# Performance work log

Measured on AMD Instinct MI355X. Metric: run time of the kernel, lower is better.

## Reference

```python
import jax, jax.numpy as jnp
import numpy as np

HEADS = 8
HEAD_DIM = 16
SCALE = HEAD_DIM ** -0.5
FIRE_RATE = 0.5
C = 128      # channel_n == embed_dim
MLP = 512


def layer_norm(x, s, b, eps=1e-5):
    m = jnp.mean(x, axis=-1, keepdims=True)
    v = jnp.mean((x - m) ** 2, axis=-1, keepdims=True)
    return (x - m) / jnp.sqrt(v + eps) * s + b


def pos_enc(H, W, D):
    # positional_encoding_3d(height, width, depth, dim=2): dim=2 path
    ph = jnp.arange(H, dtype=jnp.float32)
    pw = jnp.arange(W, dtype=jnp.float32)
    pd = jnp.arange(D, dtype=jnp.float32)
    # div terms: exp(0*-ln1e4/2)=1, exp(1*-ln1e4/2)=1e-2, exp(2*-ln1e4/2)=1e-4
    pe_h = jnp.stack([jnp.sin(ph * 1.0), jnp.cos(ph * 1.0)], -1)[:, None, None, :]
    pe_w = jnp.stack([jnp.sin(pw * 1e-2), jnp.cos(pw * 1e-2)], -1)[None, :, None, :]
    pe_d = jnp.stack([jnp.sin(pd * 1e-4), jnp.cos(pd * 1e-4)], -1)[None, None, :, :]
    return (pe_h + pe_w + pe_d).reshape(1, H * W * D, 2)


def localize(t, H, W, D):
    # t: [b, h, n, hd] -> gather zero-padded 3x3x3 neighbourhood -> [b, h, n, 27, hd]
    b, h, n, hd = t.shape
    v = t.reshape(b, h, H, W, D, hd)
    v = jnp.pad(v, ((0, 0), (0, 0), (1, 1), (1, 1), (1, 1), (0, 0)))
    shifts = [v[:, :, i:i + H, j:j + W, k:k + D, :]
              for i in range(3) for j in range(3) for k in range(3)]
    return jnp.stack(shifts, axis=-2).reshape(b, h, n, 27, hd)


def nca_step(x, params, key):
    (W_qkv, W_out, b_out, ln1_s, ln1_b, W_ff1, b_ff1, W_ff2, b_ff2,
     ln2_s, ln2_b, ln3_s, ln3_b, W_head, b_head) = params
    b, H, W, D, c = x.shape
    N = H * W * D
    xf = x.reshape(b, N, c)
    # overwrite last 2 channels with positional encoding
    pe = pos_enc(H, W, D)
    y = jnp.concatenate([xf[..., :-2], jnp.broadcast_to(pe, (b, N, 2))], axis=-1)
    # PreNorm localized attention
    yn = layer_norm(y, ln1_s, ln1_b)
    qkv = yn @ W_qkv                       # [b, N, 3*inner]
    q, k, v = jnp.split(qkv, 3, axis=-1)
    split = lambda t: t.reshape(b, N, HEADS, HEAD_DIM).transpose(0, 2, 1, 3)
    q, k, v = split(q), split(k), split(v)
    kl = localize(k, H, W, D)              # [b, h, N, 27, hd]
    vl = localize(v, H, W, D)
    dots = jnp.einsum('bhnd,bhnkd->bhnk', q, kl) * SCALE
    attn = jax.nn.softmax(dots, axis=-1)
    o = jnp.einsum('bhnk,bhnkd->bhnd', attn, vl)
    o = o.transpose(0, 2, 1, 3).reshape(b, N, HEADS * HEAD_DIM)
    y = o @ W_out + b_out + y
    # PreNorm feed-forward
    yn2 = layer_norm(y, ln2_s, ln2_b)
    ff = jax.nn.gelu(yn2 @ W_ff1 + b_ff1, approximate=False) @ W_ff2 + b_ff2
    y = ff + y
    # mlp head -> dx
    dx = layer_norm(y, ln3_s, ln3_b) @ W_head + b_head
    dx = dx.reshape(b, H, W, D, c)
    mask = (jax.random.uniform(key, (b, H, W, D, 1)) > FIRE_RATE).astype(x.dtype)
    return x + dx * mask


def setup_inputs() -> dict:
    key = jax.random.key(0)
    ks = jax.random.split(key, 8)
    s = 0.02
    inner = HEADS * HEAD_DIM
    return {
        'x': jax.random.normal(ks[0], (1, 24, 24, 24, C), jnp.float32),
        'W_qkv': jax.random.normal(ks[1], (C, 3 * inner), jnp.float32) * s,
        'W_out': jax.random.normal(ks[2], (inner, C), jnp.float32) * s,
        'b_out': jnp.zeros((C,), jnp.float32),
        'ln1_s': jnp.ones((C,), jnp.float32),
        'ln1_b': jnp.zeros((C,), jnp.float32),
        'W_ff1': jax.random.normal(ks[3], (C, MLP), jnp.float32) * s,
        'b_ff1': jnp.zeros((MLP,), jnp.float32),
        'W_ff2': jax.random.normal(ks[4], (MLP, C), jnp.float32) * s,
        'b_ff2': jnp.zeros((C,), jnp.float32),
        'ln2_s': jnp.ones((C,), jnp.float32),
        'ln2_b': jnp.zeros((C,), jnp.float32),
        'ln3_s': jnp.ones((C,), jnp.float32),
        'ln3_b': jnp.zeros((C,), jnp.float32),
        'W_head': jax.random.normal(ks[5], (C, C), jnp.float32) * s,
        'b_head': jnp.zeros((C,), jnp.float32),
        'steps': 2,
    }


def reference(x, W_qkv, W_out, b_out, ln1_s, ln1_b, W_ff1, b_ff1, W_ff2, b_ff2,
              ln2_s, ln2_b, ln3_s, ln3_b, W_head, b_head, steps):
    params = (W_qkv, W_out, b_out, ln1_s, ln1_b, W_ff1, b_ff1, W_ff2, b_ff2,
              ln2_s, ln2_b, ln3_s, ln3_b, W_head, b_head)
    key = jax.random.key(42)
    for s in range(steps):
        x = nca_step(x, params, jax.random.fold_in(key, s))
    return x
```

## Files before the change

### kernel.cpp

```cpp
#include <hip/hip_runtime.h>
#include <hip/hip_fp16.h>
#include <cstdint>
#include <cstddef>

#define NCELL 13824

typedef short bf16x8 __attribute__((ext_vector_type(8)));
typedef float f32x4  __attribute__((ext_vector_type(4)));
typedef _Float16 h2v __attribute__((ext_vector_type(2)));

__device__ __forceinline__ unsigned short f2bf(float x) {
  union { float f; uint32_t u; } c; c.f = x;
  uint32_t r = c.u + 0x7fffu + ((c.u >> 16) & 1u);
  return (unsigned short)(r >> 16);
}

__device__ __forceinline__ bf16x8 afrag_f32(const float* p) {
  float4 u0 = *(const float4*)p;
  float4 u1 = *(const float4*)(p + 4);
  bf16x8 a;
  a[0] = (short)f2bf(u0.x); a[1] = (short)f2bf(u0.y);
  a[2] = (short)f2bf(u0.z); a[3] = (short)f2bf(u0.w);
  a[4] = (short)f2bf(u1.x); a[5] = (short)f2bf(u1.y);
  a[6] = (short)f2bf(u1.z); a[7] = (short)f2bf(u1.w);
  return a;
}

__device__ __forceinline__ void ldh2x2(const __half* p, __half2& a, __half2& b) {
  uint2 u = *(const uint2*)p;
  union { uint32_t u; __half2 h; } c0, c1;
  c0.u = u.x; c1.u = u.y;
  a = c0.h; b = c1.h;
}

__device__ __forceinline__ float fdot2(__half2 a, __half2 b, float c) {
#if __has_builtin(__builtin_amdgcn_fdot2)
  union { __half2 h; h2v n; } ua, ub;
  ua.h = a; ub.h = b;
  return __builtin_amdgcn_fdot2(ua.n, ub.n, c, false);
#else
  __half2 d = __hmul2(a, b);
  return c + __low2float(d) + __high2float(d);
#endif
}

__device__ __forceinline__ float gelu_f(float x) {
  float u = 0.7978845608f * x * (1.f + 0.044715f * x * x);
  float e = __expf(2.f * u);
  float t = 1.f - 2.f / (e + 1.f);
  return 0.5f * x * (1.f + t);
}

__device__ __forceinline__ void tf2x32(uint32_t k0, uint32_t k1,
                                       uint32_t x0, uint32_t x1,
                                       uint32_t& o0, uint32_t& o1) {
  uint32_t k2 = k0 ^ k1 ^ 0x1BD11BDAu;
  x0 += k0; x1 += k1;
#define TFR(r) { x0 += x1; x1 = (x1 << (r)) | (x1 >> (32 - (r))); x1 ^= x0; }
  TFR(13) TFR(15) TFR(26) TFR(6)   x0 += k1; x1 += k2 + 1u;
  TFR(17) TFR(29) TFR(16) TFR(24)  x0 += k2; x1 += k0 + 2u;
  TFR(13) TFR(15) TFR(26) TFR(6)   x0 += k0; x1 += k1 + 3u;
  TFR(17) TFR(29) TFR(16) TFR(24)  x0 += k1; x1 += k2 + 4u;
  TFR(13) TFR(15) TFR(26) TFR(6)   x0 += k2; x1 += k0 + 5u;
#undef TFR
  o0 = x0; o1 = x1;
}

__device__ __forceinline__ float pe_val(int n, int c) {
  int dd = n % 24, ww = (n / 24) % 24, hh = n / 576;
  if (c == 126)
    return sinf((float)hh) + sinf(0.01f * (float)ww) + sinf(0.0001f * (float)dd);
  return cosf((float)hh) + cosf(0.01f * (float)ww) + cosf(0.0001f * (float)dd);
}

__device__ __forceinline__ void packOne(const float* __restrict__ W, int K, int N,
                                        unsigned short* __restrict__ P, int f) {
  int KT = K >> 5;
  int lane = f & 63;
  int ft = f >> 6;
  int kt = ft % KT, nt = ft / KT;
  int col = nt * 16 + (lane & 15);
  int k0 = kt * 32 + (lane >> 4) * 8;
  uint32_t w[4];
  #pragma unroll
  for (int p = 0; p < 4; ++p) {
    uint32_t lo = f2bf(W[(size_t)(k0 + 2 * p) * N + col]);
    uint32_t hi = f2bf(W[(size_t)(k0 + 2 * p + 1) * N + col]);
    w[p] = lo | (hi << 16);
  }
  uint4 v; v.x = w[0]; v.y = w[1]; v.z = w[2]; v.w = w[3];
  ((uint4*)P)[f] = v;
}

__global__ __launch_bounds__(256) void packAll(
    const float* __restrict__ Wqkv, const float* __restrict__ Wout,
    const float* __restrict__ Wff1, const float* __restrict__ Wff2,
    const float* __restrict__ Whead,
    unsigned short* __restrict__ pQkv, unsigned short* __restrict__ pOut,
    unsigned short* __restrict__ pFF1, unsigned short* __restrict__ pFF2,
    unsigned short* __restrict__ pHead) {
  int f = blockIdx.x * 256 + threadIdx.x;
  if (f < 6144)        packOne(Wqkv, 128, 384, pQkv, f);
  else if (f < 8192)   packOne(Wout, 128, 128, pOut, f - 6144);
  else if (f < 16384)  packOne(Wff1, 128, 512, pFF1, f - 8192);
  else if (f < 24576)  packOne(Wff2, 512, 128, pFF2, f - 16384);
  else if (f < 26624)  packOne(Whead, 128, 128, pHead, f - 24576);
}

__global__ __launch_bounds__(256) void nca_k1(
    const float* __restrict__ x, const float* __restrict__ ln1s,
    const float* __restrict__ ln1b, const unsigned short* __restrict__ pQkv,
    __half* __restrict__ wqkv,
    const int* __restrict__ steps, int s) {
  if (s >= *steps) return;
  __shared__ float ly[16][132];
  __shared__ float lmean[16], lrstd[16];
  const int t = threadIdx.x;
  const int swz = (blockIdx.x & 7) * 108 + (blockIdx.x >> 3);
  const int base = swz * 16;
  #pragma unroll
  for (int i = 0; i < 8; ++i) {
    int idx = i * 256 + t;
    int r = idx >> 7, c = idx & 127;
    int n = base + r;
    ly[r][c] = (c < 126) ? x[(size_t)n * 128 + c] : pe_val(n, c);
  }
  __syncthreads();
  { int r = t >> 4, j = t & 15;
    float s1 = 0.f, s2 = 0.f;
    #pragma unroll
    for (int cc = 0; cc < 8; ++cc) { float v = ly[r][j * 8 + cc]; s1 += v; s2 += v * v; }
    #pragma unroll
    for (int off = 1; off < 16; off <<= 1) { s1 += __shfl_xor(s1, off); s2 += __shfl_xor(s2, off); }
    if (j == 0) {
      float m = s1 * (1.f / 128.f);
      float var = s2 * (1.f / 128.f) - m * m;
      lmean[r] = m; lrstd[r] = rsqrtf(var + 1e-5f);
    }
  }
  __syncthreads();
  #pragma unroll
  for (int i = 0; i < 8; ++i) {
    int idx = i * 256 + t;
    int r = idx >> 7, c = idx & 127;
    ly[r][c] = (ly[r][c] - lmean[r]) * lrstd[r] * ln1s[c] + ln1b[c];
  }
  __syncthreads();
  const int w = t >> 6, l = t & 63;
  bf16x8 a4[4];
  #pragma unroll
  for (int kt = 0; kt < 4; ++kt)
    a4[kt] = afrag_f32(&ly[l & 15][kt * 32 + (l >> 4) * 8]);
  const bf16x8* B = (const bf16x8*)pQkv;
  #pragma unroll
  for (int q = 0; q < 6; ++q) {
    f32x4 acc = (f32x4){0.f, 0.f, 0.f, 0.f};
    int nt = w * 6 + q;
    #pragma unroll
    for (int kt = 0; kt < 4; ++kt)
      acc = __builtin_amdgcn_mfma_f32_16x16x32_bf16(a4[kt], B[(nt * 4 + kt) * 64 + l], acc, 0, 0, 0);
    int col = nt * 16 + (l & 15);
    #pragma unroll
    for (int j = 0; j < 4; ++j)
      wqkv[(size_t)(base + (l >> 4) * 4 + j) * 384 + col] = __float2half(acc[j]);
  }
}

__global__ __launch_bounds__(512, 4) void nca_kA(
    const __half* __restrict__ qkv, __half* __restrict__ qkvN,
    const unsigned short* __restrict__ pQkv,
    const unsigned short* __restrict__ pOut, const float* __restrict__ bout,
    const float* __restrict__ ln1s, const float* __restrict__ ln1b,
    const float* __restrict__ ln2s, const float* __restrict__ ln2b,
    const unsigned short* __restrict__ pFF1, const float* __restrict__ bff1,
    const unsigned short* __restrict__ pFF2, const float* __restrict__ bff2,
    const float* __restrict__ ln3s, const float* __restrict__ ln3b,
    const unsigned short* __restrict__ pHead, const float* __restrict__ bhead,
    const float* __restrict__ xin, float* __restrict__ xout,
    const int* __restrict__ steps, int s) {
  if (s >= *steps) return;
  __shared__ unsigned short lnorm[16][136];
  __shared__ float ly2[16][132];
  __shared__ unsigned short lh[16][520];
  __shared__ float lmask[16];
  const int t = threadIdx.x;
  const int swz = (blockIdx.x & 7) * 108 + (blockIdx.x >> 3);
  const int base = swz * 16;
  const int w = t >> 6, l = t & 63;
  const int lr = (l >> 4) * 4, lc = l & 15;

  float xres[4];
  {
    int col = w * 16 + lc;
    #pragma unroll
    for (int j = 0; j < 4; ++j)
      xres[j] = xin[(size_t)(base + lr + j) * 128 + col];
  }
  if (t < 16) {
    uint32_t kk0, kk1, b0, b1;
    tf2x32(0u, 42u, 0u, (uint32_t)s, kk0, kk1);
    tf2x32(kk0, kk1, 0u, (uint32_t)(base + t), b0, b1);
    uint32_t bits = b0 ^ b1;
    lmask[t] = ((bits >> 9) > 0x400000u) ? 1.0f : 0.0f;
  }
  {
    const int cell = t >> 5, head = (t >> 2) & 7, qr = t & 3;
    const int n = base + cell;
    const int dd = n % 24, ww = (n / 24) % 24, hh = n / 576;
    const int qoff = head * 16 + qr * 4;
    __half2 q0, q1;
    ldh2x2(qkv + (size_t)n * 384 + qoff, q0, q1);
    const __half* kb = qkv + 128 + qoff;
    const __half2 hz = __float2half2_rn(0.f);
    float den = 0.f;
    __half2 av0 = hz, av1 = hz;
    #pragma unroll
    for (int di = -1; di <= 1; ++di) {
      int hh2 = hh + di;
      bool okh = (unsigned)hh2 < 24u;
      int hc = min(max(hh2, 0), 23) * 576;
      #pragma unroll
      for (int dj = -1; dj <= 1; ++dj) {
        int ww2 = ww + dj;
        bool okw = okh && ((unsigned)ww2 < 24u);
        int wc = hc + min(max(ww2, 0), 23) * 24;
        #pragma unroll
        for (int dk = -1; dk <= 1; ++dk) {
          int dd2 = dd + dk;
          bool ok = okw && ((unsigned)dd2 < 24u);
          int nn = wc + min(max(dd2, 0), 23);
          const __half* kp = kb + (size_t)nn * 384;
          __half2 k0, k1, v0, v1;
          ldh2x2(kp, k0, k1);
          ldh2x2(kp + 128, v0, v1);
          float dotc = fdot2(q1, k1, fdot2(q0, k0, 0.f));
          float dot = ok ? dotc : 0.f;
          dot += __shfl_xor(dot, 1);
          dot += __shfl_xor(dot, 2);
          float e = __expf(dot * 0.25f);
          den += e;
          float em = ok ? e : 0.f;
          __half2 e2 = __float2half2_rn(em);
          av0 = __hfma2(e2, v0, av0);
          av1 = __hfma2(e2, v1, av1);
        }
      }
    }
    float inv = 1.f / den;
    float2 f0 = __half22float2(av0), f1 = __half22float2(av1);
    uint32_t w0 = (uint32_t)f2bf(f0.x * inv) | ((uint32_t)f2bf(f0.y * inv) << 16);
    uint32_t w1 = (uint32_t)f2bf(f1.x * inv) | ((uint32_t)f2bf(f1.y * inv) << 16);
    *(uint2*)&lnorm[cell][qoff] = (uint2){w0, w1};
  }
  __syncthreads();
  bf16x8 a4[4];
  #pragma unroll
  for (int kt = 0; kt < 4; ++kt)
    a4[kt] = *(const bf16x8*)&lnorm[l & 15][kt * 32 + (l >> 4) * 8];
  {
    f32x4 acc = (f32x4){0.f,0.f,0.f,0.f};
    const bf16x8* B = (const bf16x8*)pOut;
    #pragma unroll
    for (int kt = 0; kt < 4; ++kt)
      acc = __builtin_amdgcn_mfma_f32_16x16x32_bf16(a4[kt], B[(w * 4 + kt) * 64 + l], acc, 0, 0, 0);
    int col = w * 16 + lc;
    #pragma unroll
    for (int j = 0; j < 4; ++j) {
      int r = lr + j, n = base + r;
      float resy = (col < 126) ? xres[j] : pe_val(n, col);
      ly2[r][col] = acc[j] + bout[col] + resy;
    }
  }
  __syncthreads();
  {
    int r = t >> 5, j = t & 31;
    float v0 = ly2[r][j*4], v1 = ly2[r][j*4+1], v2 = ly2[r][j*4+2], v3 = ly2[r][j*4+3];
    float s1 = v0 + v1 + v2 + v3;
    float s2 = v0*v0 + v1*v1 + v2*v2 + v3*v3;
    #pragma unroll
    for (int off = 1; off < 32; off <<= 1) { s1 += __shfl_xor(s1, off); s2 += __shfl_xor(s2, off); }
    float m = s1 * (1.f / 128.f);
    float rstd = rsqrtf(s2 * (1.f / 128.f) - m * m + 1e-5f);
    float n0 = (v0 - m) * rstd * ln2s[j*4]   + ln2b[j*4];
    float n1 = (v1 - m) * rstd * ln2s[j*4+1] + ln2b[j*4+1];
    float n2 = (v2 - m) * rstd * ln2s[j*4+2] + ln2b[j*4+2];
    float n3 = (v3 - m) * rstd * ln2s[j*4+3] + ln2b[j*4+3];
    uint32_t w0 = (uint32_t)f2bf(n0) | ((uint32_t)f2bf(n1) << 16);
    uint32_t w1 = (uint32_t)f2bf(n2) | ((uint32_t)f2bf(n3) << 16);
    *(uint2*)&lnorm[r][j * 4] = (uint2){w0, w1};
  }
  __syncthreads();
  #pragma unroll
  for (int kt = 0; kt < 4; ++kt)
    a4[kt] = *(const bf16x8*)&lnorm[l & 15][kt * 32 + (l >> 4) * 8];
  {
    f32x4 acc[4];
    #pragma unroll
    for (int q = 0; q < 4; ++q) acc[q] = (f32x4){0.f,0.f,0.f,0.f};
    const bf16x8* B = (const bf16x8*)pFF1;
    #pragma unroll
    for (int kt = 0; kt < 4; ++kt) {
      #pragma unroll
      for (int q = 0; q < 4; ++q) {
        int nt = w * 4 + q;
        acc[q] = __builtin_amdgcn_mfma_f32_16x16x32_bf16(a4[kt], B[(nt * 4 + kt) * 64 + l], acc[q], 0, 0, 0);
      }
    }
    #pragma unroll
    for (int q = 0; q < 4; ++q) {
      int col = (w * 4 + q) * 16 + lc;
      #pragma unroll
      for (int j = 0; j < 4; ++j)
        lh[lr + j][col] = f2bf(gelu_f(acc[q][j] + bff1[col]));
    }
  }
  __syncthreads();
  {
    f32x4 acc = (f32x4){0.f,0.f,0.f,0.f};
    const bf16x8* B = (const bf16x8*)pFF2;
    #pragma unroll
    for (int kt = 0; kt < 16; ++kt) {
      bf16x8 a = *(const bf16x8*)&lh[l & 15][kt * 32 + (l >> 4) * 8];
      acc = __builtin_amdgcn_mfma_f32_16x16x32_bf16(a, B[(w * 16 + kt) * 64 + l], acc, 0, 0, 0);
    }
    int col = w * 16 + lc;
    #pragma unroll
    for (int j = 0; j < 4; ++j) {
      int r = lr + j;
      ly2[r][col] = acc[j] + bff2[col] + ly2[r][col];
    }
  }
  __syncthreads();
  {
    int r = t >> 5, j = t & 31;
    float v0 = ly2[r][j*4], v1 = ly2[r][j*4+1], v2 = ly2[r][j*4+2], v3 = ly2[r][j*4+3];
    float s1 = v0 + v1 + v2 + v3;
    float s2 = v0*v0 + v1*v1 + v2*v2 + v3*v3;
    #pragma unroll
    for (int off = 1; off < 32; off <<= 1) { s1 += __shfl_xor(s1, off); s2 += __shfl_xor(s2, off); }
    float m = s1 * (1.f / 128.f);
    float rstd = rsqrtf(s2 * (1.f / 128.f) - m * m + 1e-5f);
    float n0 = (v0 - m) * rstd * ln3s[j*4]   + ln3b[j*4];
    float n1 = (v1 - m) * rstd * ln3s[j*4+1] + ln3b[j*4+1];
    float n2 = (v2 - m) * rstd * ln3s[j*4+2] + ln3b[j*4+2];
    float n3 = (v3 - m) * rstd * ln3s[j*4+3] + ln3b[j*4+3];
    uint32_t w0 = (uint32_t)f2bf(n0) | ((uint32_t)f2bf(n1) << 16);
    uint32_t w1 = (uint32_t)f2bf(n2) | ((uint32_t)f2bf(n3) << 16);
    *(uint2*)&lnorm[r][j * 4] = (uint2){w0, w1};
  }
  __syncthreads();
  #pragma unroll
  for (int kt = 0; kt < 4; ++kt)
    a4[kt] = *(const bf16x8*)&lnorm[l & 15][kt * 32 + (l >> 4) * 8];
  {
    f32x4 acc = (f32x4){0.f,0.f,0.f,0.f};
    const bf16x8* B = (const bf16x8*)pHead;
    #pragma unroll
    for (int kt = 0; kt < 4; ++kt)
      acc = __builtin_amdgcn_mfma_f32_16x16x32_bf16(a4[kt], B[(w * 4 + kt) * 64 + l], acc, 0, 0, 0);
    int col = w * 16 + lc;
    #pragma unroll
    for (int j = 0; j < 4; ++j) {
      int r = lr + j;
      size_t n = base + r;
      float dx = acc[j] + bhead[col];
      float xn = xres[j] + dx * lmask[r];
      xout[n * 128 + col] = xn;
      ly2[r][col] = xn;
    }
  }
  if (s + 1 < *steps) {
    __syncthreads();
    if (t < 32) { int r = t >> 1, c = 126 + (t & 1); ly2[r][c] = pe_val(base + r, c); }
    __syncthreads();
    {
      int r = t >> 5, j = t & 31;
      float v0 = ly2[r][j*4], v1 = ly2[r][j*4+1], v2 = ly2[r][j*4+2], v3 = ly2[r][j*4+3];
      float s1 = v0 + v1 + v2 + v3;
      float s2 = v0*v0 + v1*v1 + v2*v2 + v3*v3;
      #pragma unroll
      for (int off = 1; off < 32; off <<= 1) { s1 += __shfl_xor(s1, off); s2 += __shfl_xor(s2, off); }
      float m = s1 * (1.f / 128.f);
      float rstd = rsqrtf(s2 * (1.f / 128.f) - m * m + 1e-5f);
      float n0 = (v0 - m) * rstd * ln1s[j*4]   + ln1b[j*4];
      float n1 = (v1 - m) * rstd * ln1s[j*4+1] + ln1b[j*4+1];
      float n2 = (v2 - m) * rstd * ln1s[j*4+2] + ln1b[j*4+2];
      float n3 = (v3 - m) * rstd * ln1s[j*4+3] + ln1b[j*4+3];
      uint32_t w0 = (uint32_t)f2bf(n0) | ((uint32_t)f2bf(n1) << 16);
      uint32_t w1 = (uint32_t)f2bf(n2) | ((uint32_t)f2bf(n3) << 16);
      *(uint2*)&lnorm[r][j * 4] = (uint2){w0, w1};
    }
    __syncthreads();
    #pragma unroll
    for (int kt = 0; kt < 4; ++kt)
      a4[kt] = *(const bf16x8*)&lnorm[l & 15][kt * 32 + (l >> 4) * 8];
    const bf16x8* B = (const bf16x8*)pQkv;
    #pragma unroll
    for (int q = 0; q < 3; ++q) {
      f32x4 acc = (f32x4){0.f,0.f,0.f,0.f};
      int nt = w * 3 + q;
      #pragma unroll
      for (int kt = 0; kt < 4; ++kt)
        acc = __builtin_amdgcn_mfma_f32_16x16x32_bf16(a4[kt], B[(nt * 4 + kt) * 64 + l], acc, 0, 0, 0);
      int col = nt * 16 + lc;
      #pragma unroll
      for (int j = 0; j < 4; ++j)
        qkvN[(size_t)(base + lr + j) * 384 + col] = __float2half(acc[j]);
    }
  }
}

extern "C" void kernel_launch(void* const* d_in, const int* in_sizes, int n_in,
                              void* d_out, int out_size, void* d_ws, size_t ws_size,
                              hipStream_t stream) {
  const float* x0   = (const float*)d_in[0];
  const float* Wqkv = (const float*)d_in[1];
  const float* Wout = (const float*)d_in[2];
  const float* bout = (const float*)d_in[3];
  const float* ln1s = (const float*)d_in[4];
  const float* ln1b = (const float*)d_in[5];
  const float* Wff1 = (const float*)d_in[6];
  const float* bff1 = (const float*)d_in[7];
  const float* Wff2 = (const float*)d_in[8];
  const float* bff2 = (const float*)d_in[9];
  const float* ln2s = (const float*)d_in[10];
  const float* ln2b = (const float*)d_in[11];
  const float* ln3s = (const float*)d_in[12];
  const float* ln3b = (const float*)d_in[13];
  const float* Whead= (const float*)d_in[14];
  const float* bhead= (const float*)d_in[15];
  const int*   steps= (const int*)d_in[16];
  float* out = (float*)d_out;

  __half* qkvA = (__half*)d_ws;
  __half* qkvB = qkvA + (size_t)NCELL * 384;
  unsigned short* pQkv = (unsigned short*)(qkvB + (size_t)NCELL * 384);
  unsigned short* pOut = pQkv + 128 * 384;
  unsigned short* pFF1 = pOut + 128 * 128;
  unsigned short* pFF2 = pFF1 + 128 * 512;
  unsigned short* pHead= pFF2 + 512 * 128;

  packAll<<<dim3(104), dim3(256), 0, stream>>>(Wqkv, Wout, Wff1, Wff2, Whead,
                                               pQkv, pOut, pFF1, pFF2, pHead);
  nca_k1<<<dim3(864), dim3(256), 0, stream>>>(x0, ln1s, ln1b, pQkv, qkvA, steps, 0);
  nca_kA<<<dim3(864), dim3(512), 0, stream>>>(qkvA, qkvB, pQkv, pOut, bout,
                                              ln1s, ln1b, ln2s, ln2b, pFF1, bff1,
                                              pFF2, bff2, ln3s, ln3b, pHead, bhead,
                                              x0, out, steps, 0);
  nca_kA<<<dim3(864), dim3(512), 0, stream>>>(qkvB, qkvA, pQkv, pOut, bout,
                                              ln1s, ln1b, ln2s, ln2b, pFF1, bff1,
                                              pFF2, bff2, ln3s, ln3b, pHead, bhead,
                                              out, out, steps, 1);
}
```

Baseline: 104.2 us.

## Split attention neighbours across quad lanes and precompute neighbour offset table

Changes the localized attention work split: each of the four lanes for a (cell, head) now handles 7 of the 27 neighbours over the full 16-dim head, instead of 4 dims over all 27 neighbours. A shared-memory table holds neighbour offsets and validity masks, built once per block. Partial sums of the denominator and the weighted values are combined with shuffles at the end. Each neighbour needs only one 16-byte-wide load pair instead of 27 narrow loads, and the per-neighbour shuffles go away. The cost is an extra barrier, more registers (eight accumulators), and pre-scaling q in fp16.

```diff
diff --git a/kernel.cpp b/kernel.cpp
--- a/kernel.cpp
+++ b/kernel.cpp
@@ -26,13 +26,6 @@
   return a;
 }
 
-__device__ __forceinline__ void ldh2x2(const __half* p, __half2& a, __half2& b) {
-  uint2 u = *(const uint2*)p;
-  union { uint32_t u; __half2 h; } c0, c1;
-  c0.u = u.x; c1.u = u.y;
-  a = c0.h; b = c1.h;
-}
-
 __device__ __forceinline__ float fdot2(__half2 a, __half2 b, float c) {
 #if __has_builtin(__builtin_amdgcn_fdot2)
   union { __half2 h; h2v n; } ua, ub;
@@ -42,6 +35,12 @@
   __half2 d = __hmul2(a, b);
   return c + __low2float(d) + __high2float(d);
 #endif
+}
+
+__device__ __forceinline__ __half2 shflx(__half2 v, int m) {
+  union { __half2 h; int i; } c; c.h = v;
+  c.i = __shfl_xor(c.i, m);
+  return c.h;
 }
 
 __device__ __forceinline__ float gelu_f(float x) {
@@ -182,6 +181,7 @@
   __shared__ unsigned short lnorm[16][136];
   __shared__ float ly2[16][132];
   __shared__ unsigned short lh[16][520];
+  __shared__ float4 ltab[16][28];
   __shared__ float lmask[16];
   const int t = threadIdx.x;
   const int swz = (blockIdx.x & 7) * 108 + (blockIdx.x >> 3);
@@ -203,54 +203,79 @@
     uint32_t bits = b0 ^ b1;
     lmask[t] = ((bits >> 9) > 0x400000u) ? 1.0f : 0.0f;
   }
+  if ((t & 31) < 28) {
+    int cell = t >> 5, j = t & 31;
+    int n = base + cell;
+    int dd = n % 24, ww = (n / 24) % 24, hh = n / 576;
+    bool real = j < 27;
+    int jj = real ? j : 13;
+    int di = jj / 9 - 1, dj2 = (jj / 3) % 3 - 1, dk = jj % 3 - 1;
+    int h2 = hh + di, w2 = ww + dj2, d2 = dd + dk;
+    bool ok = ((unsigned)h2 < 24u) && ((unsigned)w2 < 24u) && ((unsigned)d2 < 24u);
+    int nn = min(max(h2, 0), 23) * 576 + min(max(w2, 0), 23) * 24 + min(max(d2, 0), 23);
+    float4 e4;
+    e4.x = __int_as_float(nn * 768);
+    e4.y = real ? 1.f : 0.f;
+    e4.z = (real && ok) ? 1.f : 0.f;
+    e4.w = 0.f;
+    ltab[cell][j] = e4;
+  }
+  __syncthreads();
   {
     const int cell = t >> 5, head = (t >> 2) & 7, qr = t & 3;
     const int n = base + cell;
-    const int dd = n % 24, ww = (n / 24) % 24, hh = n / 576;
-    const int qoff = head * 16 + qr * 4;
-    __half2 q0, q1;
-    ldh2x2(qkv + (size_t)n * 384 + qoff, q0, q1);
-    const __half* kb = qkv + 128 + qoff;
+    const __half2* qp = (const __half2*)(qkv + (size_t)n * 384 + head * 16);
+    const __half2 qs = __float2half2_rn(0.25f);
+    __half2 q0 = __hmul2(qp[0], qs), q1 = __hmul2(qp[1], qs),
+            q2 = __hmul2(qp[2], qs), q3 = __hmul2(qp[3], qs),
+            q4 = __hmul2(qp[4], qs), q5 = __hmul2(qp[5], qs),
+            q6 = __hmul2(qp[6], qs), q7 = __hmul2(qp[7], qs);
+    const char* kvb = (const char*)qkv + 256 + head * 32;
+    const float4* tp = &ltab[cell][qr * 7];
     const __half2 hz = __float2half2_rn(0.f);
     float den = 0.f;
-    __half2 av0 = hz, av1 = hz;
-    #pragma unroll
-    for (int di = -1; di <= 1; ++di) {
-      int hh2 = hh + di;
-      bool okh = (unsigned)hh2 < 24u;
-      int hc = min(max(hh2, 0), 23) * 576;
-      #pragma unroll
-      for (int dj = -1; dj <= 1; ++dj) {
-        int ww2 = ww + dj;
-        bool okw = okh && ((unsigned)ww2 < 24u);
-        int wc = hc + min(max(ww2, 0), 23) * 24;
-        #pragma unroll
-        for (int dk = -1; dk <= 1; ++dk) {
-          int dd2 = dd + dk;
-          bool ok = okw && ((unsigned)dd2 < 24u);
-          int nn = wc + min(max(dd2, 0), 23);
-          const __half* kp = kb + (size_t)nn * 384;
-          __half2 k0, k1, v0, v1;
-          ldh2x2(kp, k0, k1);
-          ldh2x2(kp + 128, v0, v1);
-          float dotc = fdot2(q1, k1, fdot2(q0, k0, 0.f));
-          float dot = ok ? dotc : 0.f;
-          dot += __shfl_xor(dot, 1);
-          dot += __shfl_xor(dot, 2);
-          float e = __expf(dot * 0.25f);
-          den += e;
-          float em = ok ? e : 0.f;
-          __half2 e2 = __float2half2_rn(em);
-          av0 = __hfma2(e2, v0, av0);
-          av1 = __hfma2(e2, v1, av1);
-        }
-      }
-    }
-    float inv = 1.f / den;
-    float2 f0 = __half22float2(av0), f1 = __half22float2(av1);
+    __half2 av0=hz,av1=hz,av2=hz,av3=hz,av4=hz,av5=hz,av6=hz,av7=hz;
+    #pragma unroll
+    for (int i = 0; i < 7; ++i) {
+      float4 e4 = tp[i];
+      const char* p = kvb + __float_as_int(e4.x);
+      uint4 ka = *(const uint4*)p;
+      uint4 kb2 = *(const uint4*)(p + 16);
+      uint4 va = *(const uint4*)(p + 256);
+      uint4 vb = *(const uint4*)(p + 272);
+      union { uint32_t u; __half2 h; } c;
+      float dotc = 0.f;
+      c.u = ka.x;  dotc = fdot2(q0, c.h, dotc);
+      c.u = ka.y;  dotc = fdot2(q1, c.h, dotc);
+      c.u = ka.z;  dotc = fdot2(q2, c.h, dotc);
+      c.u = ka.w;  dotc = fdot2(q3, c.h, dotc);
+      c.u = kb2.x; dotc = fdot2(q4, c.h, dotc);
+      c.u = kb2.y; dotc = fdot2(q5, c.h, dotc);
+      c.u = kb2.z; dotc = fdot2(q6, c.h, dotc);
+      c.u = kb2.w; dotc = fdot2(q7, c.h, dotc);
+      float e = __expf(dotc * e4.z);
+      den = fmaf(e, e4.y, den);
+      __half2 ew = __float2half2_rn(e * e4.z);
+      c.u = va.x; av0 = __hfma2(ew, c.h, av0);
+      c.u = va.y; av1 = __hfma2(ew, c.h, av1);
+      c.u = va.z; av2 = __hfma2(ew, c.h, av2);
+      c.u = va.w; av3 = __hfma2(ew, c.h, av3);
+      c.u = vb.x; av4 = __hfma2(ew, c.h, av4);
+      c.u = vb.y; av5 = __hfma2(ew, c.h, av5);
+      c.u = vb.z; av6 = __hfma2(ew, c.h, av6);
+      c.u = vb.w; av7 = __hfma2(ew, c.h, av7);
+    }
+    den += __shfl_xor(den, 1); den += __shfl_xor(den, 2);
+#define CMB(v) { v = __hadd2(v, shflx(v, 1)); v = __hadd2(v, shflx(v, 2)); }
+    CMB(av0) CMB(av1) CMB(av2) CMB(av3) CMB(av4) CMB(av5) CMB(av6) CMB(av7)
+#undef CMB
+    float inv = __builtin_amdgcn_rcpf(den);
+    __half2 r0 = (qr == 0) ? av0 : (qr == 1) ? av2 : (qr == 2) ? av4 : av6;
+    __half2 r1 = (qr == 0) ? av1 : (qr == 1) ? av3 : (qr == 2) ? av5 : av7;
+    float2 f0 = __half22float2(r0), f1 = __half22float2(r1);
     uint32_t w0 = (uint32_t)f2bf(f0.x * inv) | ((uint32_t)f2bf(f0.y * inv) << 16);
     uint32_t w1 = (uint32_t)f2bf(f1.x * inv) | ((uint32_t)f2bf(f1.y * inv) << 16);
-    *(uint2*)&lnorm[cell][qoff] = (uint2){w0, w1};
+    *(uint2*)&lnorm[cell][head * 16 + qr * 4] = (uint2){w0, w1};
   }
   __syncthreads();
   bf16x8 a4[4];
```

Result: slower. 124.7 us (+19.7%).
